# Optimization experiments

Hardware: AMD Instinct MI355X
Metric: run time of the kernel (lower is better)

Reference implementation:

```python
import jax, jax.numpy as jnp
import numpy as np

N, E, D_IN, D_OUT, MAX_DEG = 50000, 800000, 128, 128, 64
ALPHA = 0.5


def _linear_params(key, fan_in, fan_out):
    s = 1.0 / np.sqrt(fan_in)
    kw, kb = jax.random.split(key)
    W = jax.random.uniform(kw, (fan_out, fan_in), jnp.float32, -s, s)
    b = jax.random.uniform(kb, (fan_out,), jnp.float32, -s, s)
    return W, b


def setup_inputs() -> dict:
    key = jax.random.key(0)
    ks = jax.random.split(key, 16)
    x = jax.random.normal(ks[0], (N, D_IN), jnp.float32)
    edge_index = jax.random.randint(ks[1], (2, E), 0, N, dtype=jnp.int64)
    in_degree = jax.random.randint(ks[2], (N,), 0, MAX_DEG, dtype=jnp.int64)
    out_degree = jax.random.randint(ks[3], (N,), 0, MAX_DEG, dtype=jnp.int64)
    out_deg_mask = jax.random.uniform(ks[4], (N,), jnp.float32)
    out_deg_mask_bias = jax.random.uniform(ks[5], (N,), jnp.float32)
    in_deg_mask = jax.random.uniform(ks[6], (N,), jnp.float32)
    in_deg_mask_bias = jax.random.uniform(ks[7], (N,), jnp.float32)
    W_src, b_src = _linear_params(ks[8], D_IN, D_OUT)
    W_dst, b_dst = _linear_params(ks[9], D_IN, D_OUT)
    W_out_f, b_out_f = _linear_params(ks[10], D_IN, 1)
    W_in_f, b_in_f = _linear_params(ks[11], D_IN, 1)
    W_fc, b_fc = _linear_params(ks[12], D_IN, D_OUT)
    # degree embedding tables, padding_idx=0 -> row 0 zeroed
    in_deg_table = (jax.random.normal(ks[13], (MAX_DEG, D_IN), jnp.float32)).at[0].set(0.0)
    out_deg_table = (jax.random.normal(ks[14], (MAX_DEG, D_IN), jnp.float32)).at[0].set(0.0)
    return {
        "x": x, "edge_index": edge_index,
        "in_degree": in_degree, "out_degree": out_degree,
        "out_deg_mask": out_deg_mask, "out_deg_mask_bias": out_deg_mask_bias,
        "in_deg_mask": in_deg_mask, "in_deg_mask_bias": in_deg_mask_bias,
        "W_src": W_src, "b_src": b_src, "W_dst": W_dst, "b_dst": b_dst,
        "W_out_f": W_out_f, "b_out_f": b_out_f, "W_in_f": W_in_f, "b_in_f": b_in_f,
        "W_fc": W_fc, "b_fc": b_fc,
        "in_deg_table": in_deg_table, "out_deg_table": out_deg_table,
    }


def reference(x, edge_index, in_degree, out_degree,
              out_deg_mask, out_deg_mask_bias, in_deg_mask, in_deg_mask_bias,
              W_src, b_src, W_dst, b_dst,
              W_out_f, b_out_f, W_in_f, b_in_f,
              W_fc, b_fc, in_deg_table, out_deg_table):
    n = x.shape[0]
    row, col = edge_index[0], edge_index[1]
    ones = jnp.ones(row.shape[0], x.dtype)
    # directed norm D_out^{-1/2} A D_in^{-1/2}; transpose reuses the same edge weights
    out_deg = jax.ops.segment_sum(ones, row, num_segments=n)
    in_deg = jax.ops.segment_sum(ones, col, num_segments=n)
    o_inv = jnp.where(out_deg > 0, jax.lax.rsqrt(jnp.maximum(out_deg, 1e-12)), 0.0)
    i_inv = jnp.where(in_deg > 0, jax.lax.rsqrt(jnp.maximum(in_deg, 1e-12)), 0.0)
    w = o_inv[row] * i_inv[col]  # [E]
    # adj_norm @ x and adj_t_norm @ x (SpMM via gather + segment_sum)
    out_nei = jax.ops.segment_sum(w[:, None] * x[col], row, num_segments=n)  # [N,D]
    in_nei = jax.ops.segment_sum(w[:, None] * x[row], col, num_segments=n)   # [N,D]
    # degree-gated filter
    c_out = (out_nei - x + out_deg_table[out_degree]) @ W_out_f.T + b_out_f  # [N,1]
    c_in = (in_nei - x + in_deg_table[in_degree]) @ W_in_f.T + b_in_f        # [N,1]
    C = jax.nn.softmax(jnp.concatenate([c_out, c_in], axis=1), axis=1)        # tau_softmax, tau=1
    C_out = C[:, 0:1] * out_deg_mask[:, None] + out_deg_mask_bias[:, None]
    C_in = C[:, 1:2] * in_deg_mask[:, None] + in_deg_mask_bias[:, None]
    out = (C_out * (out_nei @ W_src.T + b_src)
           + C_in * (in_nei @ W_dst.T + b_dst)
           + ALPHA * (x @ W_fc.T + b_fc))
    return out, C_in, C_out
```

## Files before the change

kernel.cpp:

```cpp
#include <hip/hip_runtime.h>

#define NN 50000
#define EE 800000
#define DD 128
#define CAP 48
#define MT 64
#define XSL 6250
#define PB 128

typedef short short8_t __attribute__((ext_vector_type(8)));
typedef float f32x4 __attribute__((ext_vector_type(4)));

__device__ __forceinline__ unsigned short f2bf(float f) {
    union { float f; unsigned int i; } v; v.f = f;
    unsigned int x = v.i;
    x += 0x7FFFu + ((x >> 16) & 1u);
    return (unsigned short)(x >> 16);
}
__device__ __forceinline__ unsigned int pack2(float a, float b) {
    return (unsigned int)f2bf(a) | ((unsigned int)f2bf(b) << 16);
}
__device__ __forceinline__ float2 bf2x2(unsigned int u) {
    union { unsigned int i; float f; } lo, hi;
    lo.i = u << 16;
    hi.i = u & 0xFFFF0000u;
    return make_float2(lo.f, hi.f);
}

__global__ void k_conv(const float* __restrict__ x,
                       const float* __restrict__ W_src,
                       const float* __restrict__ W_dst,
                       const float* __restrict__ W_fc,
                       unsigned short* __restrict__ xb,
                       unsigned short* __restrict__ wbf) {
    int t = blockIdx.x * 256 + threadIdx.x;
    int base = t * 4;
    if (base < NN * DD) {
        float4 v = *(const float4*)(x + base);
        uint2 p; p.x = pack2(v.x, v.y); p.y = pack2(v.z, v.w);
        *(uint2*)(xb + base) = p;
    } else {
        int b2 = base - NN * DD;
        if (b2 < 3 * 16384) {
            int src = b2 >> 14;
            int off = b2 & 16383;
            const float* W = (src == 0) ? W_src : (src == 1) ? W_dst : W_fc;
            float sc = (src == 2) ? 0.5f : 1.0f;
            float4 v = *(const float4*)(W + off);
            uint2 p; p.x = pack2(v.x * sc, v.y * sc); p.y = pack2(v.z * sc, v.w * sc);
            *(uint2*)(wbf + b2) = p;
        }
    }
}

__global__ void __launch_bounds__(256) k_place(
    const int* __restrict__ ei, int* __restrict__ cnt,
    unsigned short* __restrict__ bkt_row, unsigned short* __restrict__ bkt_col) {
    int xcd = blockIdx.x & 7;
    int b   = blockIdx.x >> 3;
    int lo = xcd * XSL, hi = lo + XSL;
    for (int e = b * 256 + threadIdx.x; e < EE; e += PB * 256) {
        int r = ei[e];
        int c = ei[EE + e];
        if (r >= lo && r < hi) {
            int po = atomicAdd(&cnt[r], 1);
            if (po < CAP) bkt_row[(size_t)r * CAP + po] = (unsigned short)c;
        }
        if (c >= lo && c < hi) {
            int pi = atomicAdd(&cnt[NN + c], 1);
            if (pi < CAP) bkt_col[(size_t)c * CAP + pi] = (unsigned short)r;
        }
    }
}

__global__ void k_inv(const int* __restrict__ cnt, float* __restrict__ inv) {
    int t = blockIdx.x * 256 + threadIdx.x;
    if (t >= 2 * NN) return;
    int d = cnt[t];
    inv[t] = (d > 0) ? (1.0f / sqrtf((float)d)) : 0.0f;
}

__global__ void __launch_bounds__(256) k_gather(
    const uint2* __restrict__ xb2, const float4* __restrict__ x4,
    const unsigned short* __restrict__ bkt_row, const unsigned short* __restrict__ bkt_col,
    const int* __restrict__ cnt,
    const float* __restrict__ o_inv, const float* __restrict__ i_inv,
    const int* __restrict__ in_degree, const int* __restrict__ out_degree,
    const float* __restrict__ odm, const float* __restrict__ odmb,
    const float* __restrict__ idm, const float* __restrict__ idmb,
    const float4* __restrict__ W_out_f4, const float* __restrict__ b_out_f,
    const float4* __restrict__ W_in_f4, const float* __restrict__ b_in_f,
    const float4* __restrict__ in_tab4, const float4* __restrict__ out_tab4,
    uint2* __restrict__ onb2, uint2* __restrict__ inb2,
    float* __restrict__ scbuf,
    float* __restrict__ outCin, float* __restrict__ outCout)
{
    __shared__ float4 sred[2][4][32];
    __shared__ float sg[2][2];
    __shared__ float sC[2][2];
    int half = threadIdx.x >> 7;
    int n = blockIdx.x * 2 + half;
    int t = threadIdx.x & 127;
    int g = t >> 5;
    int l = t & 31;
    int dir = g >> 1;
    int gd  = g & 1;

    const unsigned short* bp = ((dir == 0) ? bkt_row : bkt_col) + (size_t)n * CAP;
    const float* wnb = (dir == 0) ? i_inv : o_inv;
    int deg = cnt[dir * NN + n]; deg = (deg > CAP) ? CAP : deg;

    float4 acc = make_float4(0.f, 0.f, 0.f, 0.f);
    int j = gd;
    for (; j + 14 < deg; j += 16) {
        int nb0 = bp[j],      nb1 = bp[j + 2],  nb2_ = bp[j + 4],  nb3 = bp[j + 6];
        int nb4 = bp[j + 8],  nb5 = bp[j + 10], nb6 = bp[j + 12],  nb7 = bp[j + 14];
        float w0 = wnb[nb0], w1 = wnb[nb1], w2 = wnb[nb2_], w3 = wnb[nb3];
        float w4 = wnb[nb4], w5 = wnb[nb5], w6 = wnb[nb6],  w7 = wnb[nb7];
        uint2 u0 = xb2[(size_t)nb0 * 32 + l];
        uint2 u1 = xb2[(size_t)nb1 * 32 + l];
        uint2 u2 = xb2[(size_t)nb2_ * 32 + l];
        uint2 u3 = xb2[(size_t)nb3 * 32 + l];
        uint2 u4 = xb2[(size_t)nb4 * 32 + l];
        uint2 u5 = xb2[(size_t)nb5 * 32 + l];
        uint2 u6 = xb2[(size_t)nb6 * 32 + l];
        uint2 u7 = xb2[(size_t)nb7 * 32 + l];
        float2 p0 = bf2x2(u0.x), p1 = bf2x2(u0.y);
        float2 q0 = bf2x2(u1.x), q1 = bf2x2(u1.y);
        float2 r0 = bf2x2(u2.x), r1 = bf2x2(u2.y);
        float2 s0 = bf2x2(u3.x), s1 = bf2x2(u3.y);
        float2 t0 = bf2x2(u4.x), t1 = bf2x2(u4.y);
        float2 v0 = bf2x2(u5.x), v1 = bf2x2(u5.y);
        float2 y0 = bf2x2(u6.x), y1 = bf2x2(u6.y);
        float2 z0 = bf2x2(u7.x), z1 = bf2x2(u7.y);
        acc.x += w0 * p0.x + w1 * q0.x + w2 * r0.x + w3 * s0.x
               + w4 * t0.x + w5 * v0.x + w6 * y0.x + w7 * z0.x;
        acc.y += w0 * p0.y + w1 * q0.y + w2 * r0.y + w3 * s0.y
               + w4 * t0.y + w5 * v0.y + w6 * y0.y + w7 * z0.y;
        acc.z += w0 * p1.x + w1 * q1.x + w2 * r1.x + w3 * s1.x
               + w4 * t1.x + w5 * v1.x + w6 * y1.x + w7 * z1.x;
        acc.w += w0 * p1.y + w1 * q1.y + w2 * r1.y + w3 * s1.y
               + w4 * t1.y + w5 * v1.y + w6 * y1.y + w7 * z1.y;
    }
    for (; j + 6 < deg; j += 8) {
        int nb0 = bp[j], nb1 = bp[j + 2], nb2_ = bp[j + 4], nb3 = bp[j + 6];
        float w0 = wnb[nb0], w1 = wnb[nb1], w2 = wnb[nb2_], w3 = wnb[nb3];
        uint2 u0 = xb2[(size_t)nb0 * 32 + l];
        uint2 u1 = xb2[(size_t)nb1 * 32 + l];
        uint2 u2 = xb2[(size_t)nb2_ * 32 + l];
        uint2 u3 = xb2[(size_t)nb3 * 32 + l];
        float2 p0 = bf2x2(u0.x), p1 = bf2x2(u0.y);
        float2 q0 = bf2x2(u1.x), q1 = bf2x2(u1.y);
        float2 r0 = bf2x2(u2.x), r1 = bf2x2(u2.y);
        float2 s0 = bf2x2(u3.x), s1 = bf2x2(u3.y);
        acc.x += w0 * p0.x + w1 * q0.x + w2 * r0.x + w3 * s0.x;
        acc.y += w0 * p0.y + w1 * q0.y + w2 * r0.y + w3 * s0.y;
        acc.z += w0 * p1.x + w1 * q1.x + w2 * r1.x + w3 * s1.x;
        acc.w += w0 * p1.y + w1 * q1.y + w2 * r1.y + w3 * s1.y;
    }
    for (; j + 2 < deg; j += 4) {
        int nb0 = bp[j], nb1 = bp[j + 2];
        float w0 = wnb[nb0], w1 = wnb[nb1];
        uint2 u0 = xb2[(size_t)nb0 * 32 + l];
        uint2 u1 = xb2[(size_t)nb1 * 32 + l];
        float2 p0 = bf2x2(u0.x), p1 = bf2x2(u0.y);
        float2 q0 = bf2x2(u1.x), q1 = bf2x2(u1.y);
        acc.x += w0 * p0.x + w1 * q0.x;
        acc.y += w0 * p0.y + w1 * q0.y;
        acc.z += w0 * p1.x + w1 * q1.x;
        acc.w += w0 * p1.y + w1 * q1.y;
    }
    if (j < deg) {
        int nb = bp[j];
        float w = wnb[nb];
        uint2 u = xb2[(size_t)nb * 32 + l];
        float2 p0 = bf2x2(u.x), p1 = bf2x2(u.y);
        acc.x += w * p0.x; acc.y += w * p0.y; acc.z += w * p1.x; acc.w += w * p1.y;
    }

    sred[half][g][l] = acc;
    __syncthreads();

    float4 r = make_float4(0.f, 0.f, 0.f, 0.f);
    if (gd == 0) {
        float4 a0 = sred[half][dir * 2][l];
        float4 a1 = sred[half][dir * 2 + 1][l];
        float wn = (dir == 0) ? o_inv[n] : i_inv[n];
        r.x = wn * (a0.x + a1.x);
        r.y = wn * (a0.y + a1.y);
        r.z = wn * (a0.z + a1.z);
        r.w = wn * (a0.w + a1.w);
        float4 xv = x4[(size_t)n * 32 + l];
        float4 tb, wf;
        if (dir == 0) {
            int odg = out_degree[n];
            odg = (odg < 0) ? 0 : (odg > 63 ? 63 : odg);
            tb = out_tab4[(size_t)odg * 32 + l];
            wf = W_out_f4[l];
        } else {
            int idg = in_degree[n];
            idg = (idg < 0) ? 0 : (idg > 63 ? 63 : idg);
            tb = in_tab4[(size_t)idg * 32 + l];
            wf = W_in_f4[l];
        }
        float p = (r.x - xv.x + tb.x) * wf.x + (r.y - xv.y + tb.y) * wf.y
                + (r.z - xv.z + tb.z) * wf.z + (r.w - xv.w + tb.w) * wf.w;
        #pragma unroll
        for (int off = 16; off > 0; off >>= 1) p += __shfl_down(p, off);
        if (l == 0) sg[half][dir] = p;
    }
    __syncthreads();
    if (t == 0) {
        float c_out = sg[half][0] + b_out_f[0];
        float c_in  = sg[half][1] + b_in_f[0];
        float m  = fmaxf(c_out, c_in);
        float eo = expf(c_out - m);
        float e2 = expf(c_in  - m);
        float inv = 1.0f / (eo + e2);
        float Cout = (eo * inv) * odm[n] + odmb[n];
        float Cin  = (e2 * inv) * idm[n] + idmb[n];
        sC[half][0] = Cout; sC[half][1] = Cin;
        scbuf[2 * n]     = Cout;
        scbuf[2 * n + 1] = Cin;
        outCout[n] = Cout;
        outCin[n]  = Cin;
    }
    __syncthreads();
    if (gd == 0) {
        float C = sC[half][dir];
        uint2 pw; pw.x = pack2(C * r.x, C * r.y); pw.y = pack2(C * r.z, C * r.w);
        ((dir == 0) ? onb2 : inb2)[(size_t)n * 32 + l] = pw;
    }
}

__global__ void __launch_bounds__(256) k_gemm(
    const unsigned int* __restrict__ xb32,
    const unsigned int* __restrict__ onb32, const unsigned int* __restrict__ inb32,
    const unsigned short* __restrict__ wbf,
    const float* __restrict__ b_src, const float* __restrict__ b_dst,
    const float* __restrict__ b_fc,
    const float* __restrict__ scbuf,
    float* __restrict__ out)
{
    __shared__ unsigned short sA[MT * 72];
    __shared__ unsigned short sBt[DD * 72];

    int tid = threadIdx.x;
    int wid = tid >> 6;
    int lane = tid & 63;
    int ml = lane & 15;
    int kq = lane >> 4;
    int n0 = blockIdx.x * MT;

    f32x4 accv[8];
    #pragma unroll
    for (int i = 0; i < 8; i++) accv[i] = (f32x4)0.0f;

    const unsigned int* srcs[3] = { onb32, inb32, xb32 };

    for (int kt = 0; kt < 6; kt++) {
        int srcsel = kt >> 1;
        int k0 = (kt & 1) * 64;
        const unsigned int* S = srcs[srcsel];

        #pragma unroll
        for (int r = 0; r < 2; r++) {
            int s = tid + 256 * r;
            int row = s >> 3;
            int cg = s & 7;
            int gn = n0 + row;
            uint4 p = make_uint4(0u, 0u, 0u, 0u);
            if (gn < NN) {
                p = *(const uint4*)(S + (size_t)gn * 64 + (k0 >> 1) + cg * 4);
            }
            *(uint4*)(sA + row * 72 + cg * 8) = p;
        }
        #pragma unroll
        for (int r = 0; r < 4; r++) {
            int s = tid + 256 * r;
            int row = s >> 3;
            int cg = s & 7;
            uint4 w = *(const uint4*)(wbf + srcsel * 16384 + row * DD + k0 + cg * 8);
            *(uint4*)(sBt + row * 72 + cg * 8) = w;
        }
        __syncthreads();

        #pragma unroll
        for (int ks = 0; ks < 64; ks += 32) {
            short8_t a = *(const short8_t*)(sA + (16 * wid + ml) * 72 + ks + kq * 8);
            #pragma unroll
            for (int i = 0; i < 8; i++) {
                short8_t b = *(const short8_t*)(sBt + (16 * i + ml) * 72 + ks + kq * 8);
                accv[i] = __builtin_amdgcn_mfma_f32_16x16x32_bf16(a, b, accv[i], 0, 0, 0);
            }
        }
        __syncthreads();
    }

    int row_base = n0 + 16 * wid + 4 * kq;
    #pragma unroll
    for (int r = 0; r < 4; r++) {
        int row = row_base + r;
        if (row >= NN) continue;
        float Cout = scbuf[2 * row];
        float Cin  = scbuf[2 * row + 1];
        #pragma unroll
        for (int i = 0; i < 8; i++) {
            int col = 16 * i + ml;
            out[(size_t)row * DD + col] =
                accv[i][r] + Cout * b_src[col] + Cin * b_dst[col] + 0.5f * b_fc[col];
        }
    }
}

extern "C" void kernel_launch(void* const* d_in, const int* in_sizes, int n_in,
                              void* d_out, int out_size, void* d_ws, size_t ws_size,
                              hipStream_t stream) {
    const float* x    = (const float*)d_in[0];
    const int* ei     = (const int*)d_in[1];
    const int* in_degree  = (const int*)d_in[2];
    const int* out_degree = (const int*)d_in[3];
    const float* odm  = (const float*)d_in[4];
    const float* odmb = (const float*)d_in[5];
    const float* idm  = (const float*)d_in[6];
    const float* idmb = (const float*)d_in[7];
    const float* W_src = (const float*)d_in[8];
    const float* b_src = (const float*)d_in[9];
    const float* W_dst = (const float*)d_in[10];
    const float* b_dst = (const float*)d_in[11];
    const float* W_out_f = (const float*)d_in[12];
    const float* b_out_f = (const float*)d_in[13];
    const float* W_in_f  = (const float*)d_in[14];
    const float* b_in_f  = (const float*)d_in[15];
    const float* W_fc    = (const float*)d_in[16];
    const float* b_fc    = (const float*)d_in[17];
    const float* in_tab  = (const float*)d_in[18];
    const float* out_tab = (const float*)d_in[19];

    unsigned short* xb  = (unsigned short*)d_ws;
    unsigned short* onb = xb + (size_t)NN * DD;
    unsigned short* inb = onb + (size_t)NN * DD;
    float* scbuf = (float*)(inb + (size_t)NN * DD);
    float* invb  = scbuf + 2 * NN;
    unsigned short* wbf = (unsigned short*)(invb + 2 * NN);
    int* cnt     = (int*)(wbf + 3 * 16384);
    unsigned short* bkt_row = (unsigned short*)(cnt + 2 * NN);
    unsigned short* bkt_col = bkt_row + (size_t)NN * CAP;

    hipMemsetAsync(cnt, 0, (size_t)2 * NN * sizeof(int), stream);

    int conv_quads = (NN * DD + 3 * 16384) / 4;
    k_conv<<<(conv_quads + 255) / 256, 256, 0, stream>>>(x, W_src, W_dst, W_fc, xb, wbf);
    k_place<<<8 * PB, 256, 0, stream>>>(ei, cnt, bkt_row, bkt_col);
    k_inv<<<(2 * NN + 255) / 256, 256, 0, stream>>>(cnt, invb);

    float* o_inv = invb;
    float* i_inv = invb + NN;
    float* out_p  = (float*)d_out;
    float* cin_p  = out_p + (size_t)NN * DD;
    float* cout_p = cin_p + NN;

    k_gather<<<NN / 2, 256, 0, stream>>>((const uint2*)xb, (const float4*)x,
                                         bkt_row, bkt_col, cnt,
                                         o_inv, i_inv, in_degree, out_degree,
                                         odm, odmb, idm, idmb,
                                         (const float4*)W_out_f, b_out_f,
                                         (const float4*)W_in_f, b_in_f,
                                         (const float4*)in_tab, (const float4*)out_tab,
                                         (uint2*)onb, (uint2*)inb,
                                         scbuf, cin_p, cout_p);

    k_gemm<<<(NN + MT - 1) / MT, 256, 0, stream>>>(
        (const unsigned int*)xb, (const unsigned int*)onb, (const unsigned int*)inb,
        wbf, b_src, b_dst, b_fc, scbuf, out_p);
}
```

Baseline: 292.0 us.

## Prescale x by inverse in-degree and gather 16-byte rows with shuffle-broadcast indices

```diff
diff --git a/kernel.cpp b/kernel.cpp
--- a/kernel.cpp
+++ b/kernel.cpp
@@ -25,6 +25,12 @@
     lo.i = u << 16;
     hi.i = u & 0xFFFF0000u;
     return make_float2(lo.f, hi.f);
+}
+
+__device__ __forceinline__ void acc8(float4& a, float4& b, uint4 u, float w) {
+    float2 p0 = bf2x2(u.x), p1 = bf2x2(u.y), p2 = bf2x2(u.z), p3 = bf2x2(u.w);
+    a.x += w * p0.x; a.y += w * p0.y; a.z += w * p1.x; a.w += w * p1.y;
+    b.x += w * p2.x; b.y += w * p2.y; b.z += w * p3.x; b.w += w * p3.y;
 }
 
 __global__ void k_conv(const float* __restrict__ x,
@@ -73,18 +79,37 @@
     }
 }
 
-__global__ void k_inv(const int* __restrict__ cnt, float* __restrict__ inv) {
+__global__ void __launch_bounds__(256) k_prep(
+    const int* __restrict__ cnt, const float4* __restrict__ x4,
+    float* __restrict__ invb, float* __restrict__ w2, uint2* __restrict__ xs2)
+{
     int t = blockIdx.x * 256 + threadIdx.x;
-    if (t >= 2 * NN) return;
-    int d = cnt[t];
-    inv[t] = (d > 0) ? (1.0f / sqrtf((float)d)) : 0.0f;
+    if (t < 2 * NN) {
+        int d = cnt[t];
+        invb[t] = (d > 0) ? (1.0f / sqrtf((float)d)) : 0.0f;
+    }
+    if (t < NN) {
+        int dd = cnt[t];
+        int di = cnt[NN + t];
+        float o = (dd > 0) ? (1.0f / sqrtf((float)dd)) : 0.0f;
+        w2[t] = (di > 0) ? o * sqrtf((float)di) : o;
+    }
+    if (t < NN * 32) {
+        int node = t >> 5;
+        int di = cnt[NN + node];
+        float s = (di > 0) ? (1.0f / sqrtf((float)di)) : 1.0f;
+        float4 v = x4[t];
+        uint2 p; p.x = pack2(v.x * s, v.y * s); p.y = pack2(v.z * s, v.w * s);
+        xs2[t] = p;
+    }
 }
 
 __global__ void __launch_bounds__(256) k_gather(
-    const uint2* __restrict__ xb2, const float4* __restrict__ x4,
+    const uint4* __restrict__ xs4, const float4* __restrict__ x4,
     const unsigned short* __restrict__ bkt_row, const unsigned short* __restrict__ bkt_col,
     const int* __restrict__ cnt,
     const float* __restrict__ o_inv, const float* __restrict__ i_inv,
+    const float* __restrict__ w2,
     const int* __restrict__ in_degree, const int* __restrict__ out_degree,
     const float* __restrict__ odm, const float* __restrict__ odmb,
     const float* __restrict__ idm, const float* __restrict__ idmb,
@@ -95,7 +120,7 @@
     float* __restrict__ scbuf,
     float* __restrict__ outCin, float* __restrict__ outCout)
 {
-    __shared__ float4 sred[2][4][32];
+    __shared__ float4 sred[2][4][2][16][2];
     __shared__ float sg[2][2];
     __shared__ float sC[2][2];
     int half = threadIdx.x >> 7;
@@ -105,91 +130,104 @@
     int l = t & 31;
     int dir = g >> 1;
     int gd  = g & 1;
+    int sub = l >> 4;
+    int li  = l & 15;
+    int shamt = gd << 4;
 
     const unsigned short* bp = ((dir == 0) ? bkt_row : bkt_col) + (size_t)n * CAP;
-    const float* wnb = (dir == 0) ? i_inv : o_inv;
     int deg = cnt[dir * NN + n]; deg = (deg > CAP) ? CAP : deg;
 
-    float4 acc = make_float4(0.f, 0.f, 0.f, 0.f);
-    int j = gd;
-    for (; j + 14 < deg; j += 16) {
-        int nb0 = bp[j],      nb1 = bp[j + 2],  nb2_ = bp[j + 4],  nb3 = bp[j + 6];
-        int nb4 = bp[j + 8],  nb5 = bp[j + 10], nb6 = bp[j + 12],  nb7 = bp[j + 14];
-        float w0 = wnb[nb0], w1 = wnb[nb1], w2 = wnb[nb2_], w3 = wnb[nb3];
-        float w4 = wnb[nb4], w5 = wnb[nb5], w6 = wnb[nb6],  w7 = wnb[nb7];
-        uint2 u0 = xb2[(size_t)nb0 * 32 + l];
-        uint2 u1 = xb2[(size_t)nb1 * 32 + l];
-        uint2 u2 = xb2[(size_t)nb2_ * 32 + l];
-        uint2 u3 = xb2[(size_t)nb3 * 32 + l];
-        uint2 u4 = xb2[(size_t)nb4 * 32 + l];
-        uint2 u5 = xb2[(size_t)nb5 * 32 + l];
-        uint2 u6 = xb2[(size_t)nb6 * 32 + l];
-        uint2 u7 = xb2[(size_t)nb7 * 32 + l];
-        float2 p0 = bf2x2(u0.x), p1 = bf2x2(u0.y);
-        float2 q0 = bf2x2(u1.x), q1 = bf2x2(u1.y);
-        float2 r0 = bf2x2(u2.x), r1 = bf2x2(u2.y);
-        float2 s0 = bf2x2(u3.x), s1 = bf2x2(u3.y);
-        float2 t0 = bf2x2(u4.x), t1 = bf2x2(u4.y);
-        float2 v0 = bf2x2(u5.x), v1 = bf2x2(u5.y);
-        float2 y0 = bf2x2(u6.x), y1 = bf2x2(u6.y);
-        float2 z0 = bf2x2(u7.x), z1 = bf2x2(u7.y);
-        acc.x += w0 * p0.x + w1 * q0.x + w2 * r0.x + w3 * s0.x
-               + w4 * t0.x + w5 * v0.x + w6 * y0.x + w7 * z0.x;
-        acc.y += w0 * p0.y + w1 * q0.y + w2 * r0.y + w3 * s0.y
-               + w4 * t0.y + w5 * v0.y + w6 * y0.y + w7 * z0.y;
-        acc.z += w0 * p1.x + w1 * q1.x + w2 * r1.x + w3 * s1.x
-               + w4 * t1.x + w5 * v1.x + w6 * y1.x + w7 * z1.x;
-        acc.w += w0 * p1.y + w1 * q1.y + w2 * r1.y + w3 * s1.y
-               + w4 * t1.y + w5 * v1.y + w6 * y1.y + w7 * z1.y;
-    }
-    for (; j + 6 < deg; j += 8) {
-        int nb0 = bp[j], nb1 = bp[j + 2], nb2_ = bp[j + 4], nb3 = bp[j + 6];
-        float w0 = wnb[nb0], w1 = wnb[nb1], w2 = wnb[nb2_], w3 = wnb[nb3];
-        uint2 u0 = xb2[(size_t)nb0 * 32 + l];
-        uint2 u1 = xb2[(size_t)nb1 * 32 + l];
-        uint2 u2 = xb2[(size_t)nb2_ * 32 + l];
-        uint2 u3 = xb2[(size_t)nb3 * 32 + l];
-        float2 p0 = bf2x2(u0.x), p1 = bf2x2(u0.y);
-        float2 q0 = bf2x2(u1.x), q1 = bf2x2(u1.y);
-        float2 r0 = bf2x2(u2.x), r1 = bf2x2(u2.y);
-        float2 s0 = bf2x2(u3.x), s1 = bf2x2(u3.y);
-        acc.x += w0 * p0.x + w1 * q0.x + w2 * r0.x + w3 * s0.x;
-        acc.y += w0 * p0.y + w1 * q0.y + w2 * r0.y + w3 * s0.y;
-        acc.z += w0 * p1.x + w1 * q1.x + w2 * r1.x + w3 * s1.x;
-        acc.w += w0 * p1.y + w1 * q1.y + w2 * r1.y + w3 * s1.y;
-    }
-    for (; j + 2 < deg; j += 4) {
-        int nb0 = bp[j], nb1 = bp[j + 2];
-        float w0 = wnb[nb0], w1 = wnb[nb1];
-        uint2 u0 = xb2[(size_t)nb0 * 32 + l];
-        uint2 u1 = xb2[(size_t)nb1 * 32 + l];
-        float2 p0 = bf2x2(u0.x), p1 = bf2x2(u0.y);
-        float2 q0 = bf2x2(u1.x), q1 = bf2x2(u1.y);
-        acc.x += w0 * p0.x + w1 * q0.x;
-        acc.y += w0 * p0.y + w1 * q0.y;
-        acc.z += w0 * p1.x + w1 * q1.x;
-        acc.w += w0 * p1.y + w1 * q1.y;
-    }
-    if (j < deg) {
-        int nb = bp[j];
-        float w = wnb[nb];
-        uint2 u = xb2[(size_t)nb * 32 + l];
-        float2 p0 = bf2x2(u.x), p1 = bf2x2(u.y);
-        acc.x += w * p0.x; acc.y += w * p0.y; acc.z += w * p1.x; acc.w += w * p1.y;
-    }
-
-    sred[half][g][l] = acc;
+    unsigned int bw = (l < 24) ? *(const unsigned int*)(bp + 2 * l) : 0u;
+
+    float w_l = 0.0f;
+    if (dir == 1) {
+        unsigned int pr = __shfl(bw, l >> 1, 32);
+        int il = (pr >> ((l & 1) << 4)) & 0xffff;
+        if (l < deg) w_l = w2[il];
+    }
+
+    float4 ac0 = make_float4(0.f, 0.f, 0.f, 0.f);
+    float4 ac1 = make_float4(0.f, 0.f, 0.f, 0.f);
+
+    if (dir == 0 || deg <= 32) {
+        int j = gd;
+        for (; j + 14 < deg; j += 16) {
+            int s0 = j + 2 * sub, s1 = s0 + 4, s2 = s0 + 8, s3 = s0 + 12;
+            int i0 = (__shfl(bw, s0 >> 1, 32) >> shamt) & 0xffff;
+            int i1 = (__shfl(bw, s1 >> 1, 32) >> shamt) & 0xffff;
+            int i2 = (__shfl(bw, s2 >> 1, 32) >> shamt) & 0xffff;
+            int i3 = (__shfl(bw, s3 >> 1, 32) >> shamt) & 0xffff;
+            uint4 u0 = xs4[(size_t)i0 * 16 + li];
+            uint4 u1 = xs4[(size_t)i1 * 16 + li];
+            uint4 u2 = xs4[(size_t)i2 * 16 + li];
+            uint4 u3 = xs4[(size_t)i3 * 16 + li];
+            float w0 = 1.f, w1 = 1.f, w2v = 1.f, w3 = 1.f;
+            if (dir) {
+                w0  = __shfl(w_l, s0, 32);
+                w1  = __shfl(w_l, s1, 32);
+                w2v = __shfl(w_l, s2, 32);
+                w3  = __shfl(w_l, s3, 32);
+            }
+            acc8(ac0, ac1, u0, w0);
+            acc8(ac0, ac1, u1, w1);
+            acc8(ac0, ac1, u2, w2v);
+            acc8(ac0, ac1, u3, w3);
+        }
+        for (; j + 6 < deg; j += 8) {
+            int s0 = j + 2 * sub, s1 = s0 + 4;
+            int i0 = (__shfl(bw, s0 >> 1, 32) >> shamt) & 0xffff;
+            int i1 = (__shfl(bw, s1 >> 1, 32) >> shamt) & 0xffff;
+            uint4 u0 = xs4[(size_t)i0 * 16 + li];
+            uint4 u1 = xs4[(size_t)i1 * 16 + li];
+            float w0 = 1.f, w1 = 1.f;
+            if (dir) {
+                w0 = __shfl(w_l, s0, 32);
+                w1 = __shfl(w_l, s1, 32);
+            }
+            acc8(ac0, ac1, u0, w0);
+            acc8(ac0, ac1, u1, w1);
+        }
+        for (; j < deg; j += 4) {
+            int s0 = j + 2 * sub;
+            int sc = (s0 < deg) ? s0 : gd;
+            int i0 = (__shfl(bw, sc >> 1, 32) >> shamt) & 0xffff;
+            float w0 = 1.f;
+            if (dir) w0 = __shfl(w_l, sc, 32);
+            if (s0 < deg) {
+                uint4 u0 = xs4[(size_t)i0 * 16 + li];
+                acc8(ac0, ac1, u0, w0);
+            }
+        }
+    } else {
+        for (int j = gd; j < deg; j += 4) {
+            int s0 = j + 2 * sub;
+            int sc = (s0 < deg) ? s0 : gd;
+            int i0 = (__shfl(bw, sc >> 1, 32) >> shamt) & 0xffff;
+            if (s0 < deg) {
+                float w0 = w2[i0];
+                uint4 u0 = xs4[(size_t)i0 * 16 + li];
+                acc8(ac0, ac1, u0, w0);
+            }
+        }
+    }
+
+    sred[half][g][sub][li][0] = ac0;
+    sred[half][g][sub][li][1] = ac1;
     __syncthreads();
 
     float4 r = make_float4(0.f, 0.f, 0.f, 0.f);
     if (gd == 0) {
-        float4 a0 = sred[half][dir * 2][l];
-        float4 a1 = sred[half][dir * 2 + 1][l];
+        int src = l >> 1, q = l & 1;
+        int g0 = dir * 2;
+        float4 b0 = sred[half][g0][0][src][q];
+        float4 b1 = sred[half][g0][1][src][q];
+        float4 b2 = sred[half][g0 + 1][0][src][q];
+        float4 b3 = sred[half][g0 + 1][1][src][q];
         float wn = (dir == 0) ? o_inv[n] : i_inv[n];
-        r.x = wn * (a0.x + a1.x);
-        r.y = wn * (a0.y + a1.y);
-        r.z = wn * (a0.z + a1.z);
-        r.w = wn * (a0.w + a1.w);
+        r.x = wn * (b0.x + b1.x + b2.x + b3.x);
+        r.y = wn * (b0.y + b1.y + b2.y + b3.y);
+        r.z = wn * (b0.z + b1.z + b2.z + b3.z);
+        r.w = wn * (b0.w + b1.w + b2.w + b3.w);
         float4 xv = x4[(size_t)n * 32 + l];
         float4 tb, wf;
         if (dir == 0) {
@@ -340,9 +378,11 @@
     unsigned short* xb  = (unsigned short*)d_ws;
     unsigned short* onb = xb + (size_t)NN * DD;
     unsigned short* inb = onb + (size_t)NN * DD;
-    float* scbuf = (float*)(inb + (size_t)NN * DD);
+    unsigned short* xs  = inb + (size_t)NN * DD;
+    float* scbuf = (float*)(xs + (size_t)NN * DD);
     float* invb  = scbuf + 2 * NN;
-    unsigned short* wbf = (unsigned short*)(invb + 2 * NN);
+    float* w2    = invb + 2 * NN;
+    unsigned short* wbf = (unsigned short*)(w2 + NN);
     int* cnt     = (int*)(wbf + 3 * 16384);
     unsigned short* bkt_row = (unsigned short*)(cnt + 2 * NN);
     unsigned short* bkt_col = bkt_row + (size_t)NN * CAP;
@@ -352,7 +392,8 @@
     int conv_quads = (NN * DD + 3 * 16384) / 4;
     k_conv<<<(conv_quads + 255) / 256, 256, 0, stream>>>(x, W_src, W_dst, W_fc, xb, wbf);
     k_place<<<8 * PB, 256, 0, stream>>>(ei, cnt, bkt_row, bkt_col);
-    k_inv<<<(2 * NN + 255) / 256, 256, 0, stream>>>(cnt, invb);
+    k_prep<<<(NN * 32 + 255) / 256, 256, 0, stream>>>(cnt, (const float4*)x,
+                                                      invb, w2, (uint2*)xs);
 
     float* o_inv = invb;
     float* i_inv = invb + NN;
@@ -360,9 +401,9 @@
     float* cin_p  = out_p + (size_t)NN * DD;
     float* cout_p = cin_p + NN;
 
-    k_gather<<<NN / 2, 256, 0, stream>>>((const uint2*)xb, (const float4*)x,
+    k_gather<<<NN / 2, 256, 0, stream>>>((const uint4*)xs, (const float4*)x,
                                          bkt_row, bkt_col, cnt,
-                                         o_inv, i_inv, in_degree, out_degree,
+                                         o_inv, i_inv, w2, in_degree, out_degree,
                                          odm, odmb, idm, idmb,
                                          (const float4*)W_out_f, b_out_f,
                                          (const float4*)W_in_f, b_in_f,
```

Measured after the change: 285.5 us. 2.2% less time.
